# Kernel optimization log

Measured on AMD Instinct MI355X. Metric: run time of the kernel, lower is better.

Reference implementation:

```python
import jax, jax.numpy as jnp
import numpy as np

B, L, D = 4, 2048, 1024
DK, H = 64, 16
DFF = 4 * D
MASK_FILL = -2**15 + 1  # -32767, matches masked_fill value in source


def setup_inputs() -> dict:
    key = jax.random.key(0)
    ks = jax.random.split(key, 16)
    s = lambda fan_in: 1.0 / np.sqrt(fan_in)
    inp = {
        "x": jax.random.normal(ks[0], (B, L, D), dtype=jnp.float32),
        "maskPAD": jax.random.randint(ks[1], (B, L, L), 0, 2, dtype=jnp.int32),
        # attention projections (torch Linear layout: [out, in])
        "WQ_w": jax.random.uniform(ks[2], (H * DK, D), jnp.float32, -s(D), s(D)),
        "WQ_b": jnp.zeros((H * DK,), jnp.float32),
        "WK_w": jax.random.uniform(ks[3], (H * DK, D), jnp.float32, -s(D), s(D)),
        "WK_b": jnp.zeros((H * DK,), jnp.float32),
        "WV_w": jax.random.uniform(ks[4], (H * DK, D), jnp.float32, -s(D), s(D)),
        "WV_b": jnp.zeros((H * DK,), jnp.float32),
        "WO_w": jax.random.uniform(ks[5], (D, H * DK), jnp.float32, -s(H * DK), s(H * DK)),
        "WO_b": jnp.zeros((D,), jnp.float32),
        # FFN (pre-LN inside the FFN block)
        "ln_g": jnp.ones((D,), jnp.float32),
        "ln_b": jnp.zeros((D,), jnp.float32),
        "W1_w": jax.random.uniform(ks[6], (DFF, D), jnp.float32, -s(D), s(D)),
        "W1_b": jnp.zeros((DFF,), jnp.float32),
        "W2_w": jax.random.uniform(ks[7], (D, DFF), jnp.float32, -s(DFF), s(DFF)),
        "W2_b": jnp.zeros((D,), jnp.float32),
    }
    return inp


def _layernorm(x, g, b, eps=1e-5):
    mu = jnp.mean(x, axis=-1, keepdims=True)
    var = jnp.var(x, axis=-1, keepdims=True)
    return (x - mu) * jax.lax.rsqrt(var + eps) * g + b


def reference(x, maskPAD, WQ_w, WQ_b, WK_w, WK_b, WV_w, WV_b, WO_w, WO_b,
              ln_g, ln_b, W1_w, W1_b, W2_w, W2_b):
    # --- SelfAttention_PostLN (dropout = identity at eval) ---
    q = (jnp.einsum('bld,ed->ble', x, WQ_w) + WQ_b).reshape(B, L, H, DK).transpose(0, 2, 1, 3)
    k = (jnp.einsum('bld,ed->ble', x, WK_w) + WK_b).reshape(B, L, H, DK).transpose(0, 2, 1, 3)
    v = (jnp.einsum('bld,ed->ble', x, WV_w) + WV_b).reshape(B, L, H, DK).transpose(0, 2, 1, 3)
    scores = jnp.einsum('bhqd,bhkd->bhqk', q, k) / np.sqrt(DK).astype(np.float32)
    scores = jnp.where((maskPAD == 0)[:, None, :, :], jnp.float32(MASK_FILL), scores)
    alpha = jax.nn.softmax(scores, axis=-1)
    z = jnp.einsum('bhqk,bhkd->bhqd', alpha, v)  # [B,H,L,DK]
    z = z.transpose(0, 2, 1, 3).reshape(B, L, H * DK)
    z = jnp.einsum('ble,de->bld', z, WO_w) + WO_b
    # --- FFN_PreLN ---
    r = x + z                                    # residual 1 (dropout identity)
    h = _layernorm(r, ln_g, ln_b)
    h = jax.nn.relu(jnp.einsum('bld,fd->blf', h, W1_w) + W1_b)
    h = jnp.einsum('blf,df->bld', h, W2_w) + W2_b
    return r + h
```

## Files before the change

kernel.cpp:

```cpp
#include <hip/hip_runtime.h>

#define BD      4
#define LSEQ    2048
#define DMODEL  1024
#define HHEADS  16
#define DKK     64
#define DFFN    4096
#define MROWS   (BD*LSEQ)
#define QKS     2048

typedef float  f32x4  __attribute__((ext_vector_type(4)));
typedef float  f32x16 __attribute__((ext_vector_type(16)));
typedef __bf16 bf16x8 __attribute__((ext_vector_type(8)));
typedef unsigned short u16x8 __attribute__((ext_vector_type(8)));
typedef unsigned int   u32x4 __attribute__((ext_vector_type(4)));

__device__ inline unsigned short f2bf(float x) {
    union { float f; unsigned u; } c; c.f = x;
    unsigned r = c.u + 0x7FFFu + ((c.u >> 16) & 1u);
    return (unsigned short)(r >> 16);
}

__global__ void cast_bf16_k(const float* __restrict__ in,
                            unsigned short* __restrict__ out, long n) {
    long i = ((long)blockIdx.x * blockDim.x + threadIdx.x) * 4;
    long stride = (long)gridDim.x * blockDim.x * 4;
    for (; i < n; i += stride) {
        float4 v = *(const float4*)(in + i);
        ushort4 o;
        o.x = f2bf(v.x); o.y = f2bf(v.y); o.z = f2bf(v.z); o.w = f2bf(v.w);
        *(ushort4*)(out + i) = o;
    }
}

__global__ void concat3_k(const float* __restrict__ a, const float* __restrict__ b,
                          const float* __restrict__ c, float* __restrict__ o) {
    int i = blockIdx.x * 256 + threadIdx.x;
    if (i < 1024) { o[i] = a[i]; o[1024 + i] = b[i]; o[2048 + i] = c[i]; }
}

__global__ __launch_bounds__(256) void maskbits_k(const int* __restrict__ m,
                                                  unsigned long long* __restrict__ bits) {
    const long gw = ((long)blockIdx.x * blockDim.x + threadIdx.x) >> 6;
    const int lane = threadIdx.x & 63;
    const int b   = (int)(gw >> 16);
    const int rem = (int)gw & 65535;
    const int q = rem >> 5, kt = rem & 31;
    const int v = m[((size_t)(b*LSEQ + q))*LSEQ + kt*64 + lane];
    const unsigned long long bal = __ballot(v != 0);
    if (lane == 0) bits[((size_t)(b*32 + kt))*LSEQ + q] = bal;
}

__device__ inline void gload16(const void* g, void* l) {
    __builtin_amdgcn_global_load_lds(
        (const __attribute__((address_space(1))) void*)g,
        (__attribute__((address_space(3))) void*)l, 16, 0, 0);
}

#define BAR() { __builtin_amdgcn_sched_barrier(0); __builtin_amdgcn_s_barrier(); __builtin_amdgcn_sched_barrier(0); }

#define STAGE(XSEL, XPTR, h, tau, s)                                              \
  { const unsigned short* gs0 = (XPTR) + (size_t)((h)*128 + wid*8 + srow) * K + (tau)*64 + schk*8; \
    gload16(gs0, (void*)&sm[(s)][(XSEL)][(((h)*128 + wid*8)*64)]);                 \
    gload16(gs0 + (size_t)64*K, (void*)&sm[(s)][(XSEL)][(((h)*128 + 64 + wid*8)*64)]); }

#define LDA(dst, s, mi, kk) dst = *(const bf16x8*)(&sm[(s)][0][(wr*128 + (mi)*16 + r0)*64 + ((((kk)*4 + g) ^ (r0 & 7)) << 3)]);
#define LDB(dst, s, nj, kk) dst = *(const bf16x8*)(&sm[(s)][1][(wc*64  + (nj)*16 + r0)*64 + ((((kk)*4 + g) ^ (r0 & 7)) << 3)]);

#define PHASE_MFMA(q)                                                                                   \
    __builtin_amdgcn_s_setprio(1);                                                                      \
    _Pragma("unroll")                                                                                   \
    for (int nj = 0; nj < 4; ++nj) {                                                                    \
        acc[2*(q)][nj]   = __builtin_amdgcn_mfma_f32_16x16x32_bf16(af00, bq[nj][0], acc[2*(q)][nj],   0,0,0); \
        acc[2*(q)][nj]   = __builtin_amdgcn_mfma_f32_16x16x32_bf16(af01, bq[nj][1], acc[2*(q)][nj],   0,0,0); \
        acc[2*(q)+1][nj] = __builtin_amdgcn_mfma_f32_16x16x32_bf16(af10, bq[nj][0], acc[2*(q)+1][nj], 0,0,0); \
        acc[2*(q)+1][nj] = __builtin_amdgcn_mfma_f32_16x16x32_bf16(af11, bq[nj][1], acc[2*(q)+1][nj], 0,0,0); \
    }                                                                                                   \
    __builtin_amdgcn_s_setprio(0);

#define KTILE(s, tau)                                                        \
  {                                                                          \
    const int tp1 = (tau) + 1, tp2 = (tau) + 2;                              \
    bf16x8 bq[4][2];                                                         \
    bf16x8 af00, af01, af10, af11;                                           \
    _Pragma("unroll") for (int nj = 0; nj < 4; ++nj) {                       \
        LDB(bq[nj][0], s, nj, 0); LDB(bq[nj][1], s, nj, 1); }                \
    LDA(af00, s, 0, 0); LDA(af01, s, 0, 1);                                  \
    LDA(af10, s, 1, 0); LDA(af11, s, 1, 1);                                  \
    if (tp1 < NTT) { STAGE(0, Ab, 0, tp1, (s)^1); }                          \
    BAR(); PHASE_MFMA(0); BAR();                                             \
    LDA(af00, s, 2, 0); LDA(af01, s, 2, 1);                                  \
    LDA(af10, s, 3, 0); LDA(af11, s, 3, 1);                                  \
    if (tp1 < NTT) { STAGE(0, Ab, 1, tp1, (s)^1); }                          \
    if (tp2 < NTT) { STAGE(1, Bb, 0, tp2, (s)); }                            \
    BAR(); PHASE_MFMA(1); BAR();                                             \
    LDA(af00, s, 4, 0); LDA(af01, s, 4, 1);                                  \
    LDA(af10, s, 5, 0); LDA(af11, s, 5, 1);                                  \
    if (tp2 < NTT) { STAGE(1, Bb, 1, tp2, (s)); }                            \
    BAR(); PHASE_MFMA(2); BAR();                                             \
    LDA(af00, s, 6, 0); LDA(af01, s, 6, 1);                                  \
    LDA(af10, s, 7, 0); LDA(af11, s, 7, 1);                                  \
    if (tp2 < NTT)      { asm volatile("s_waitcnt vmcnt(4)" ::: "memory"); } \
    else if (tp1 < NTT) { asm volatile("s_waitcnt vmcnt(0)" ::: "memory"); } \
    BAR(); PHASE_MFMA(3); BAR();                                             \
  }

template<int MODE, int NTT>
__global__ __launch_bounds__(512, 1) void gemm8(const unsigned short* __restrict__ A,
                                                const unsigned short* __restrict__ B,
                                                const float* __restrict__ bias,
                                                unsigned short* __restrict__ Cout,
                                                int M, int N, int K, float scaleQ)
{
    __shared__ unsigned short sm[2][2][256*64];
    const int t   = threadIdx.x;
    const int wid = t >> 6, lane = t & 63;
    const int wr  = wid >> 2, wc = wid & 3;
    const int r0  = lane & 15, g = lane >> 4;

    const int nwg = gridDim.x;
    const int bid = (blockIdx.x & 7) * (nwg >> 3) + (blockIdx.x >> 3);
    const int ntn = N >> 8;
    const int bm  = (bid / ntn) << 8, bn = (bid % ntn) << 8;

    const int srow = lane >> 3;
    const int schk = (lane & 7) ^ srow;
    const unsigned short* Ab = A + (size_t)bm * K;
    const unsigned short* Bb = B + (size_t)bn * K;

    f32x4 acc[8][4] = {};

    STAGE(1, Bb, 0, 0, 0); STAGE(1, Bb, 1, 0, 0);
    STAGE(0, Ab, 0, 0, 0); STAGE(0, Ab, 1, 0, 0);
    STAGE(1, Bb, 0, 1, 1); STAGE(1, Bb, 1, 1, 1);
    asm volatile("s_waitcnt vmcnt(4)" ::: "memory");
    BAR();

#pragma unroll 1
    for (int i2 = 0; i2 < NTT/2; ++i2) {
        const int tau = 2*i2;
        KTILE(0, tau);
        KTILE(1, tau+1);
    }

#pragma unroll
    for (int mi = 0; mi < 8; ++mi) {
        const int row0 = bm + wr*128 + mi*16 + g*4;
#pragma unroll
        for (int nj = 0; nj < 4; ++nj) {
            const int col = bn + wc*64 + nj*16 + r0;
            const float bcol = bias[col];
#pragma unroll
            for (int rr = 0; rr < 4; ++rr) {
                float c = acc[mi][nj][rr] + bcol;
                if (MODE == 1) c = fmaxf(c, 0.f);
                Cout[(size_t)(row0 + rr) * N + col] = f2bf(c);
            }
        }
    }
}

#define STAGEA2(h, tau, s)                                                        \
  { const unsigned short* gs0 = Ab + (size_t)((h)*128 + wid*8 + srow) * K + (tau)*64 + schk*8; \
    gload16(gs0, (void*)&smA[(s)][(((h)*128 + wid*8)*64)]);                        \
    gload16(gs0 + (size_t)64*K, (void*)&smA[(s)][(((h)*128 + 64 + wid*8)*64)]); }

#define STAGEB2(tau, s)                                                           \
  { const unsigned short* gs0 = Bb + (size_t)(wid*8 + srow) * K + (tau)*64 + schk*8; \
    gload16(gs0, (void*)&smB[(s)][((wid*8)*64)]);                                  \
    gload16(gs0 + (size_t)64*K, (void*)&smB[(s)][((64 + wid*8)*64)]); }

#define LDA2(dst, s, mi, kk) dst = *(const bf16x8*)(&smA[(s)][(wr*128 + (mi)*16 + r0)*64 + ((((kk)*4 + g) ^ (r0 & 7)) << 3)]);
#define LDB2(dst, s, nj, kk) dst = *(const bf16x8*)(&smB[(s)][(wc*32  + (nj)*16 + r0)*64 + ((((kk)*4 + g) ^ (r0 & 7)) << 3)]);

#define PHASE_MFMA2X(q0)                                                                                \
    __builtin_amdgcn_s_setprio(1);                                                                      \
    _Pragma("unroll")                                                                                   \
    for (int mm = 0; mm < 4; ++mm) {                                                                    \
        acc[(q0)+mm][0] = __builtin_amdgcn_mfma_f32_16x16x32_bf16(aa[2*mm],   bq[0][0], acc[(q0)+mm][0], 0,0,0); \
        acc[(q0)+mm][0] = __builtin_amdgcn_mfma_f32_16x16x32_bf16(aa[2*mm+1], bq[0][1], acc[(q0)+mm][0], 0,0,0); \
        acc[(q0)+mm][1] = __builtin_amdgcn_mfma_f32_16x16x32_bf16(aa[2*mm],   bq[1][0], acc[(q0)+mm][1], 0,0,0); \
        acc[(q0)+mm][1] = __builtin_amdgcn_mfma_f32_16x16x32_bf16(aa[2*mm+1], bq[1][1], acc[(q0)+mm][1], 0,0,0); \
    }                                                                                                   \
    __builtin_amdgcn_s_setprio(0);

#define KTILE2(s, tau)                                                       \
  {                                                                          \
    const int tp1 = (tau) + 1, tp2 = (tau) + 2;                              \
    bf16x8 bq[2][2];                                                         \
    bf16x8 aa[8];                                                            \
    LDB2(bq[0][0], s, 0, 0); LDB2(bq[0][1], s, 0, 1);                        \
    LDB2(bq[1][0], s, 1, 0); LDB2(bq[1][1], s, 1, 1);                        \
    LDA2(aa[0], s, 0, 0); LDA2(aa[1], s, 0, 1);                              \
    LDA2(aa[2], s, 1, 0); LDA2(aa[3], s, 1, 1);                              \
    LDA2(aa[4], s, 2, 0); LDA2(aa[5], s, 2, 1);                              \
    LDA2(aa[6], s, 3, 0); LDA2(aa[7], s, 3, 1);                              \
    if (tp1 < NTT) { STAGEA2(0, tp1, (s)^1); }                               \
    BAR(); PHASE_MFMA2X(0); BAR();                                           \
    LDA2(aa[0], s, 4, 0); LDA2(aa[1], s, 4, 1);                              \
    LDA2(aa[2], s, 5, 0); LDA2(aa[3], s, 5, 1);                              \
    LDA2(aa[4], s, 6, 0); LDA2(aa[5], s, 6, 1);                              \
    LDA2(aa[6], s, 7, 0); LDA2(aa[7], s, 7, 1);                              \
    if (tp1 < NTT) { STAGEA2(1, tp1, (s)^1); }                               \
    if (tp2 < NTT) { STAGEB2(tp2, (s)); }                                    \
    if (tp2 < NTT)      { asm volatile("s_waitcnt vmcnt(2)" ::: "memory"); } \
    else if (tp1 < NTT) { asm volatile("s_waitcnt vmcnt(0)" ::: "memory"); } \
    BAR(); PHASE_MFMA2X(4); BAR();                                           \
  }

template<int MODE, int NTT>
__global__ __launch_bounds__(512, 1) void gemm8n(const unsigned short* __restrict__ A,
                                                 const unsigned short* __restrict__ B,
                                                 const float* __restrict__ bias,
                                                 const float* __restrict__ resid,
                                                 void* __restrict__ Cout,
                                                 unsigned short* __restrict__ vt,
                                                 int M, int N, int K, float scaleQ)
{
    __shared__ unsigned short smA[2][256*64];
    __shared__ unsigned short smB[2][128*64];
    const int t   = threadIdx.x;
    const int wid = t >> 6, lane = t & 63;
    const int wr  = wid >> 2, wc = wid & 3;
    const int r0  = lane & 15, g = lane >> 4;

    const int nwg = gridDim.x;
    const int bid = (blockIdx.x & 7) * (nwg >> 3) + (blockIdx.x >> 3);
    const int ntn = N >> 7;
    const int bm  = (bid / ntn) << 8, bn = (bid % ntn) << 7;

    const int srow = lane >> 3;
    const int schk = (lane & 7) ^ srow;
    const unsigned short* Ab = A + (size_t)bm * K;
    const unsigned short* Bb = B + (size_t)bn * K;

    f32x4 acc[8][2] = {};

    STAGEB2(0, 0);
    STAGEA2(0, 0, 0); STAGEA2(1, 0, 0);
    STAGEB2(1, 1);
    asm volatile("s_waitcnt vmcnt(2)" ::: "memory");
    BAR();

#pragma unroll 1
    for (int i2 = 0; i2 < NTT/2; ++i2) {
        const int tau = 2*i2;
        KTILE2(0, tau);
        KTILE2(1, tau+1);
    }

#pragma unroll
    for (int mi = 0; mi < 8; ++mi) {
        const int row0 = bm + wr*128 + mi*16 + g*4;
#pragma unroll
        for (int nj = 0; nj < 2; ++nj) {
            const int col = bn + wc*32 + nj*16 + r0;
            const float bcol = bias[col];
#pragma unroll
            for (int rr = 0; rr < 4; ++rr) {
                const int row = row0 + rr;
                if (MODE == 2) {
                    float c = acc[mi][nj][rr] + bcol;
                    ((float*)Cout)[(size_t)row * N + col] = c + resid[(size_t)row * N + col];
                }
            }
            if (MODE == 3) {
                if (col < 2048) {
                    const float sc = (col < 1024) ? scaleQ : 1.0f;
#pragma unroll
                    for (int rr = 0; rr < 4; ++rr)
                        ((unsigned short*)Cout)[(size_t)(row0 + rr) * QKS + col] =
                            f2bf((acc[mi][nj][rr] + bcol) * sc);
                } else {
                    const int vcol = col - 2048;
                    const int b = row0 >> 11, tok = row0 & 2047;
                    ushort4 h4;
                    h4.x = f2bf(acc[mi][nj][0] + bcol);
                    h4.y = f2bf(acc[mi][nj][1] + bcol);
                    h4.z = f2bf(acc[mi][nj][2] + bcol);
                    h4.w = f2bf(acc[mi][nj][3] + bcol);
                    *(ushort4*)&vt[((size_t)(b*1024 + vcol))*LSEQ + tok] = h4;
                }
            }
        }
    }
}

#define MFILL   (-47272.79f)
#define DEFTHR  (11.5415603f)
__global__ __launch_bounds__(256, 3) void attn_k(
    const unsigned short* __restrict__ QK,
    const unsigned short* __restrict__ VT,
    const unsigned long long* __restrict__ MBits,
    unsigned short* __restrict__ Z)
{
    __shared__ unsigned short Ks[2][64*64];
    __shared__ unsigned short Vs[2][64*64];
    __shared__ float Sc[4*32];

    const int t    = threadIdx.x;
    const int w    = t >> 6, lane = t & 63;
    const int q31  = lane & 31, hi = lane >> 5;

    const int bid = blockIdx.x;
    const int sw  = (bid & 7) * 128 + (bid >> 3);
    const int qt  = sw & 15, h = (sw >> 4) & 15, b = sw >> 8;
    const int qw  = qt * 128 + w * 32;

    const unsigned short* Qg = QK + ((size_t)(b*LSEQ + qw + q31))*QKS + h*DKK + hi*8;
    bf16x8 qf[4];
#pragma unroll
    for (int ds = 0; ds < 4; ++ds)
        qf[ds] = *(const bf16x8*)(Qg + ds*16);

    const int srow = w*8 + (lane>>3);
    const int schk = (lane & 7) ^ (srow & 7);
    const unsigned short* kP = QK + ((size_t)(b*LSEQ))*QKS + 1024 + h*DKK
                                  + (size_t)srow*QKS + schk*8;
    const unsigned short* vP = VT + ((size_t)(b*1024 + h*DKK))*LSEQ
                                  + (size_t)srow*LSEQ + schk*8;
    const unsigned long long* mP = MBits + ((size_t)(b*32))*LSEQ + (qw + q31);

    float m_r = MFILL, l_r = 0.f;
    f32x16 z0, z1;
#pragma unroll
    for (int r = 0; r < 16; ++r) { z0[r] = 0.f; z1[r] = 0.f; }

    gload16(kP,           &Ks[0][w*512]);
    gload16(kP + 32*QKS,  &Ks[0][w*512] + 2048);
    gload16(vP,           &Vs[0][w*512]);
    gload16(vP + 32*LSEQ, &Vs[0][w*512] + 2048);
    unsigned long long mw = *mP;
    kP += 64*QKS; vP += 64; mP += LSEQ;

    for (int kt = 0; kt < LSEQ/64; ++kt) {
        const int cur = kt & 1;
        __syncthreads();

        gload16(kP,           &Ks[cur^1][w*512]);
        gload16(kP + 32*QKS,  &Ks[cur^1][w*512] + 2048);
        gload16(vP,           &Vs[cur^1][w*512]);
        gload16(vP + 32*LSEQ, &Vs[cur^1][w*512] + 2048);
        const unsigned long long mwn = (kt < LSEQ/64 - 1) ? *mP : mw;
        kP += 64*QKS; vP += 64; mP += LSEQ;

        const unsigned long long sh = mw >> (hi*4);
        const unsigned md0 = (unsigned)sh, md1 = (unsigned)(sh >> 32);

        f32x16 s0, s1;
#pragma unroll
        for (int r = 0; r < 16; ++r) { s0[r] = 0.f; s1[r] = 0.f; }
        __builtin_amdgcn_s_setprio(1);
#pragma unroll
        for (int ds = 0; ds < 4; ++ds) {
            const int slot = ((ds*2 + hi) ^ (q31 & 7)) << 3;
            bf16x8 kf0 = *(const bf16x8*)(&Ks[cur][ q31     *64 + slot]);
            bf16x8 kf1 = *(const bf16x8*)(&Ks[cur][(32+q31)*64 + slot]);
            s0 = __builtin_amdgcn_mfma_f32_32x32x16_bf16(kf0, qf[ds], s0, 0, 0, 0);
            s1 = __builtin_amdgcn_mfma_f32_32x32x16_bf16(kf1, qf[ds], s1, 0, 0, 0);
        }
        __builtin_amdgcn_s_setprio(0);

        float a8[16];
#pragma unroll
        for (int r = 0; r < 16; ++r) a8[r] = fmaxf(s0[r], s1[r]);
        {
            float t0 = fmaxf(fmaxf(a8[0],  a8[1]),  a8[2]);
            float t1 = fmaxf(fmaxf(a8[3],  a8[4]),  a8[5]);
            float t2 = fmaxf(fmaxf(a8[6],  a8[7]),  a8[8]);
            float t3 = fmaxf(fmaxf(a8[9],  a8[10]), a8[11]);
            float t4 = fmaxf(fmaxf(a8[12], a8[13]), a8[14]);
            float u0 = fmaxf(fmaxf(t0, t1), t2);
            float u1 = fmaxf(fmaxf(t3, t4), a8[15]);
            float tm = fmaxf(u0, u1);
            float ta = tm, tb = tm;
            asm volatile("v_permlane32_swap_b32 %0, %1" : "+v"(ta), "+v"(tb));
            tm = fmaxf(tm, hi ? ta : tb);

            if (__any(tm > m_r + DEFTHR)) {
                const float nm   = fmaxf(m_r, tm);
                const float corr = exp2f(m_r - nm);
                Sc[w*32 + q31] = corr;
                l_r *= corr;
                m_r  = nm;
#pragma unroll
                for (int r = 0; r < 16; ++r) {
                    const int row = (r & 3) + 8*(r >> 2) + 4*hi;
                    const float cr = Sc[w*32 + row];
                    z0[r] *= cr; z1[r] *= cr;
                }
            }
        }

#pragma unroll
        for (int r = 0; r < 16; ++r) {
            const int kb = (r & 3) + 8*(r >> 2);
            s0[r] = exp2f(s0[r] - m_r);
            s1[r] = exp2f(s1[r] - m_r);
            if (!((md0 >> kb) & 1)) s0[r] = 0.f;
            if (!((md1 >> kb) & 1)) s1[r] = 0.f;
        }
        float r4[8];
#pragma unroll
        for (int r = 0; r < 8; ++r)
            r4[r] = (s0[2*r] + s0[2*r+1]) + (s1[2*r] + s1[2*r+1]);
        float rs = ((r4[0]+r4[1]) + (r4[2]+r4[3])) + ((r4[4]+r4[5]) + (r4[6]+r4[7]));
        {
            float ra = rs, rb = rs;
            asm volatile("v_permlane32_swap_b32 %0, %1" : "+v"(ra), "+v"(rb));
            rs += hi ? ra : rb;
        }
        l_r += rs;

        __builtin_amdgcn_s_setprio(1);
#pragma unroll
        for (int half = 0; half < 2; ++half) {
#pragma unroll
            for (int sub = 0; sub < 2; ++sub) {
                const int base = sub*8;
                unsigned wa, wb, wc2, wd;
                float p0 = half ? s1[base+0] : s0[base+0];
                float p1 = half ? s1[base+1] : s0[base+1];
                float p2 = half ? s1[base+2] : s0[base+2];
                float p3 = half ? s1[base+3] : s0[base+3];
                float p4 = half ? s1[base+4] : s0[base+4];
                float p5 = half ? s1[base+5] : s0[base+5];
                float p6 = half ? s1[base+6] : s0[base+6];
                float p7 = half ? s1[base+7] : s0[base+7];
                asm("v_cvt_pk_bf16_f32 %0, %1, %2" : "=v"(wa) : "v"(p0), "v"(p1));
                asm("v_cvt_pk_bf16_f32 %0, %1, %2" : "=v"(wb) : "v"(p4), "v"(p5));
                asm("v_cvt_pk_bf16_f32 %0, %1, %2" : "=v"(wc2) : "v"(p2), "v"(p3));
                asm("v_cvt_pk_bf16_f32 %0, %1, %2" : "=v"(wd) : "v"(p6), "v"(p7));
                asm volatile("v_permlane32_swap_b32 %0, %1" : "+v"(wa), "+v"(wb));
                asm volatile("v_permlane32_swap_b32 %0, %1" : "+v"(wc2), "+v"(wd));
                u32x4 pu; pu[0] = wa; pu[1] = wc2; pu[2] = wb; pu[3] = wd;
                bf16x8 pa = __builtin_bit_cast(bf16x8, pu);
                const int ks = half*2 + sub;
                const int slot = ((ks*2 + hi) ^ (q31 & 7)) << 3;
                bf16x8 vf0 = *(const bf16x8*)(&Vs[cur][ q31     *64 + slot]);
                bf16x8 vf1 = *(const bf16x8*)(&Vs[cur][(32+q31)*64 + slot]);
                z0 = __builtin_amdgcn_mfma_f32_32x32x16_bf16(pa, vf0, z0, 0, 0, 0);
                z1 = __builtin_amdgcn_mfma_f32_32x32x16_bf16(pa, vf1, z1, 0, 0, 0);
            }
        }
        __builtin_amdgcn_s_setprio(0);

        mw = mwn;
    }

    Sc[w*32 + q31] = l_r;
    unsigned short* Zb = Z + ((size_t)(b*LSEQ + qw))*DMODEL + h*DKK + q31;
#pragma unroll
    for (int r = 0; r < 16; ++r) {
        const int row = (r & 3) + 8*(r >> 2) + 4*hi;
        const float rl = 1.0f / Sc[w*32 + row];
        Zb[(size_t)row*DMODEL]      = f2bf(z0[r] * rl);
        Zb[(size_t)row*DMODEL + 32] = f2bf(z1[r] * rl);
    }
}

__global__ __launch_bounds__(256) void ln_k(const float* __restrict__ r,
                                            const float* __restrict__ gam,
                                            const float* __restrict__ bet,
                                            unsigned short* __restrict__ out)
{
    const int row = blockIdx.x;
    const int t = threadIdx.x;
    const float* rp = r + (size_t)row * DMODEL;
    float4 v = *(const float4*)(rp + t*4);
    float s  = v.x + v.y + v.z + v.w;
    float s2 = v.x*v.x + v.y*v.y + v.z*v.z + v.w*v.w;
#pragma unroll
    for (int off = 32; off >= 1; off >>= 1) {
        s  += __shfl_xor(s,  off);
        s2 += __shfl_xor(s2, off);
    }
    __shared__ float red[8];
    const int wv = t >> 6;
    if ((t & 63) == 0) { red[wv] = s; red[4 + wv] = s2; }
    __syncthreads();
    s  = red[0] + red[1] + red[2] + red[3];
    s2 = red[4] + red[5] + red[6] + red[7];
    const float mu   = s  * (1.f/DMODEL);
    const float var  = s2 * (1.f/DMODEL) - mu*mu;
    const float rstd = rsqrtf(var + 1e-5f);
    float4 gv = *(const float4*)(gam + t*4);
    float4 bv = *(const float4*)(bet + t*4);
    ushort4 o;
    o.x = f2bf((v.x - mu)*rstd*gv.x + bv.x);
    o.y = f2bf((v.y - mu)*rstd*gv.y + bv.y);
    o.z = f2bf((v.z - mu)*rstd*gv.z + bv.z);
    o.w = f2bf((v.w - mu)*rstd*gv.w + bv.w);
    *(ushort4*)(out + (size_t)row * DMODEL + t*4) = o;
}

extern "C" void kernel_launch(void* const* d_in, const int* in_sizes, int n_in,
                              void* d_out, int out_size, void* d_ws, size_t ws_size,
                              hipStream_t stream)
{
    const float* x    = (const float*)d_in[0];
    const int*   mask = (const int*)  d_in[1];
    const float* WQ_w = (const float*)d_in[2];
    const float* WQ_b = (const float*)d_in[3];
    const float* WK_w = (const float*)d_in[4];
    const float* WK_b = (const float*)d_in[5];
    const float* WV_w = (const float*)d_in[6];
    const float* WV_b = (const float*)d_in[7];
    const float* WO_w = (const float*)d_in[8];
    const float* WO_b = (const float*)d_in[9];
    const float* ln_g = (const float*)d_in[10];
    const float* ln_b = (const float*)d_in[11];
    const float* W1_w = (const float*)d_in[12];
    const float* W1_b = (const float*)d_in[13];
    const float* W2_w = (const float*)d_in[14];
    const float* W2_b = (const float*)d_in[15];
    float* out = (float*)d_out;

    char* w = (char*)d_ws;
    const size_t MB = 1024*1024;
    unsigned short* qk   = (unsigned short*)(w + 0*MB);
    unsigned short* vtb  = (unsigned short*)(w + 32*MB);
    unsigned short* shr  = (unsigned short*)(w + 64*MB);
    float*          rb   = (float*)         (w + 80*MB);
    unsigned short* wqkv = (unsigned short*)(w + 112*MB);
    unsigned short* wob  = (unsigned short*)(w + 118*MB);
    unsigned short* w1b  = (unsigned short*)(w + 120*MB);
    unsigned short* w2b  = (unsigned short*)(w + 128*MB);
    unsigned long long* mbits = (unsigned long long*)(w + 136*MB);
    float* bqkv = (float*)rb;
    unsigned short* xb   = shr;
    unsigned short* Zb   = shr;
    unsigned short* hln  = shr;
    unsigned short* hmid = (unsigned short*)(w + 0*MB);

    cast_bf16_k<<<2048, 256, 0, stream>>>(x,    xb,   (long)MROWS*DMODEL);
    cast_bf16_k<<<512,  256, 0, stream>>>(WQ_w, wqkv,               (long)DMODEL*DMODEL);
    cast_bf16_k<<<512,  256, 0, stream>>>(WK_w, wqkv + 1024*1024,   (long)DMODEL*DMODEL);
    cast_bf16_k<<<512,  256, 0, stream>>>(WV_w, wqkv + 2*1024*1024, (long)DMODEL*DMODEL);
    cast_bf16_k<<<512,  256, 0, stream>>>(WO_w, wob,  (long)DMODEL*DMODEL);
    cast_bf16_k<<<2048, 256, 0, stream>>>(W1_w, w1b,  (long)DFFN*DMODEL);
    cast_bf16_k<<<2048, 256, 0, stream>>>(W2_w, w2b,  (long)DMODEL*DFFN);
    maskbits_k<<<65536, 256, 0, stream>>>(mask, mbits);
    concat3_k<<<4, 256, 0, stream>>>(WQ_b, WK_b, WV_b, bqkv);

    gemm8n<3, 16><<<dim3(768), dim3(512), 0, stream>>>(xb, wqkv, bqkv, nullptr, qk, vtb,
                                                       MROWS, 3072, DMODEL, 0.18033688f);
    attn_k<<<dim3(1024), dim3(256), 0, stream>>>(qk, vtb, mbits, Zb);
    gemm8n<2, 16><<<dim3(256), dim3(512), 0, stream>>>(Zb, wob, WO_b, x, rb, nullptr,
                                                       MROWS, DMODEL, DMODEL, 1.0f);
    ln_k<<<MROWS, 256, 0, stream>>>(rb, ln_g, ln_b, hln);
    gemm8<1, 16><<<dim3(512), dim3(512), 0, stream>>>(hln, w1b, W1_b, hmid,
                                                      MROWS, DFFN, DMODEL, 1.0f);
    gemm8n<2, 64><<<dim3(256), dim3(512), 0, stream>>>(hmid, w2b, W2_b, rb, out, nullptr,
                                                       MROWS, DMODEL, DFFN, 1.0f);
}
```

Baseline: 472.8 us.

## Merge weight casts into one kernel and move QKV/W2 GEMMs to 256x256 tiles

The six separate weight-cast launches become one grid-stride kernel that converts all weight matrices. The QKV projection and the W2 down-projection move from the 256x128-tile gemm8n kernel to the 256x256-tile gemm8 kernel, which gains the residual and QKV/V-transpose epilogues. Larger tiles raise arithmetic intensity and cut redundant operand loads. The cost is fewer workgroups: 384 for QKV and only 128 for W2, which may underfill the 256 CUs on MI355X.

After: 474.3 us. About the same (+0.3%).

```diff
diff --git a/kernel.cpp b/kernel.cpp
--- a/kernel.cpp
+++ b/kernel.cpp
@@ -30,6 +30,29 @@
         ushort4 o;
         o.x = f2bf(v.x); o.y = f2bf(v.y); o.z = f2bf(v.z); o.w = f2bf(v.w);
         *(ushort4*)(out + i) = o;
+    }
+}
+
+__global__ void cast_weights_k(const float* __restrict__ wq, const float* __restrict__ wk,
+                               const float* __restrict__ wv, const float* __restrict__ wo,
+                               const float* __restrict__ w1, const float* __restrict__ w2,
+                               unsigned short* __restrict__ dqkv, unsigned short* __restrict__ dwo,
+                               unsigned short* __restrict__ dw1, unsigned short* __restrict__ dw2) {
+    const long M1 = 1024*1024;
+    long i = ((long)blockIdx.x * blockDim.x + threadIdx.x) * 4;
+    long stride = (long)gridDim.x * blockDim.x * 4;
+    for (; i < 12*M1; i += stride) {
+        const float* src; unsigned short* dst;
+        if      (i <   M1) { src = wq + i;          dst = dqkv + i; }
+        else if (i < 2*M1) { src = wk + (i-M1);     dst = dqkv + i; }
+        else if (i < 3*M1) { src = wv + (i-2*M1);   dst = dqkv + i; }
+        else if (i < 4*M1) { src = wo + (i-3*M1);   dst = dwo + (i-3*M1); }
+        else if (i < 8*M1) { src = w1 + (i-4*M1);   dst = dw1 + (i-4*M1); }
+        else               { src = w2 + (i-8*M1);   dst = dw2 + (i-8*M1); }
+        float4 v = *(const float4*)src;
+        ushort4 o;
+        o.x = f2bf(v.x); o.y = f2bf(v.y); o.z = f2bf(v.z); o.w = f2bf(v.w);
+        *(ushort4*)dst = o;
     }
 }
 
@@ -109,7 +132,9 @@
 __global__ __launch_bounds__(512, 1) void gemm8(const unsigned short* __restrict__ A,
                                                 const unsigned short* __restrict__ B,
                                                 const float* __restrict__ bias,
-                                                unsigned short* __restrict__ Cout,
+                                                const float* __restrict__ resid,
+                                                void* __restrict__ Cout,
+                                                unsigned short* __restrict__ vt,
                                                 int M, int N, int K, float scaleQ)
 {
     __shared__ unsigned short sm[2][2][256*64];
@@ -150,11 +175,35 @@
         for (int nj = 0; nj < 4; ++nj) {
             const int col = bn + wc*64 + nj*16 + r0;
             const float bcol = bias[col];
-#pragma unroll
-            for (int rr = 0; rr < 4; ++rr) {
-                float c = acc[mi][nj][rr] + bcol;
-                if (MODE == 1) c = fmaxf(c, 0.f);
-                Cout[(size_t)(row0 + rr) * N + col] = f2bf(c);
+            if (MODE == 1) {
+#pragma unroll
+                for (int rr = 0; rr < 4; ++rr) {
+                    float c = fmaxf(acc[mi][nj][rr] + bcol, 0.f);
+                    ((unsigned short*)Cout)[(size_t)(row0 + rr) * N + col] = f2bf(c);
+                }
+            } else if (MODE == 2) {
+#pragma unroll
+                for (int rr = 0; rr < 4; ++rr) {
+                    const size_t idx = (size_t)(row0 + rr) * N + col;
+                    ((float*)Cout)[idx] = acc[mi][nj][rr] + bcol + resid[idx];
+                }
+            } else if (MODE == 3) {
+                if (col < 2048) {
+                    const float sc = (col < 1024) ? scaleQ : 1.0f;
+#pragma unroll
+                    for (int rr = 0; rr < 4; ++rr)
+                        ((unsigned short*)Cout)[(size_t)(row0 + rr) * QKS + col] =
+                            f2bf((acc[mi][nj][rr] + bcol) * sc);
+                } else {
+                    const int vcol = col - 2048;
+                    const int b = row0 >> 11, tok = row0 & 2047;
+                    ushort4 h4;
+                    h4.x = f2bf(acc[mi][nj][0] + bcol);
+                    h4.y = f2bf(acc[mi][nj][1] + bcol);
+                    h4.z = f2bf(acc[mi][nj][2] + bcol);
+                    h4.w = f2bf(acc[mi][nj][3] + bcol);
+                    *(ushort4*)&vt[((size_t)(b*1024 + vcol))*LSEQ + tok] = h4;
+                }
             }
         }
     }
@@ -214,8 +263,7 @@
                                                  const float* __restrict__ bias,
                                                  const float* __restrict__ resid,
                                                  void* __restrict__ Cout,
-                                                 unsigned short* __restrict__ vt,
-                                                 int M, int N, int K, float scaleQ)
+                                                 int M, int N, int K)
 {
     __shared__ unsigned short smA[2][256*64];
     __shared__ unsigned short smB[2][128*64];
@@ -262,24 +310,6 @@
                 if (MODE == 2) {
                     float c = acc[mi][nj][rr] + bcol;
                     ((float*)Cout)[(size_t)row * N + col] = c + resid[(size_t)row * N + col];
-                }
-            }
-            if (MODE == 3) {
-                if (col < 2048) {
-                    const float sc = (col < 1024) ? scaleQ : 1.0f;
-#pragma unroll
-                    for (int rr = 0; rr < 4; ++rr)
-                        ((unsigned short*)Cout)[(size_t)(row0 + rr) * QKS + col] =
-                            f2bf((acc[mi][nj][rr] + bcol) * sc);
-                } else {
-                    const int vcol = col - 2048;
-                    const int b = row0 >> 11, tok = row0 & 2047;
-                    ushort4 h4;
-                    h4.x = f2bf(acc[mi][nj][0] + bcol);
-                    h4.y = f2bf(acc[mi][nj][1] + bcol);
-                    h4.z = f2bf(acc[mi][nj][2] + bcol);
-                    h4.w = f2bf(acc[mi][nj][3] + bcol);
-                    *(ushort4*)&vt[((size_t)(b*1024 + vcol))*LSEQ + tok] = h4;
                 }
             }
         }
@@ -533,24 +563,20 @@
     unsigned short* hln  = shr;
     unsigned short* hmid = (unsigned short*)(w + 0*MB);
 
-    cast_bf16_k<<<2048, 256, 0, stream>>>(x,    xb,   (long)MROWS*DMODEL);
-    cast_bf16_k<<<512,  256, 0, stream>>>(WQ_w, wqkv,               (long)DMODEL*DMODEL);
-    cast_bf16_k<<<512,  256, 0, stream>>>(WK_w, wqkv + 1024*1024,   (long)DMODEL*DMODEL);
-    cast_bf16_k<<<512,  256, 0, stream>>>(WV_w, wqkv + 2*1024*1024, (long)DMODEL*DMODEL);
-    cast_bf16_k<<<512,  256, 0, stream>>>(WO_w, wob,  (long)DMODEL*DMODEL);
-    cast_bf16_k<<<2048, 256, 0, stream>>>(W1_w, w1b,  (long)DFFN*DMODEL);
-    cast_bf16_k<<<2048, 256, 0, stream>>>(W2_w, w2b,  (long)DMODEL*DFFN);
+    cast_bf16_k<<<2048, 256, 0, stream>>>(x, xb, (long)MROWS*DMODEL);
+    cast_weights_k<<<2048, 256, 0, stream>>>(WQ_w, WK_w, WV_w, WO_w, W1_w, W2_w,
+                                             wqkv, wob, w1b, w2b);
     maskbits_k<<<65536, 256, 0, stream>>>(mask, mbits);
     concat3_k<<<4, 256, 0, stream>>>(WQ_b, WK_b, WV_b, bqkv);
 
-    gemm8n<3, 16><<<dim3(768), dim3(512), 0, stream>>>(xb, wqkv, bqkv, nullptr, qk, vtb,
-                                                       MROWS, 3072, DMODEL, 0.18033688f);
+    gemm8<3, 16><<<dim3(384), dim3(512), 0, stream>>>(xb, wqkv, bqkv, nullptr, qk, vtb,
+                                                      MROWS, 3072, DMODEL, 0.18033688f);
     attn_k<<<dim3(1024), dim3(256), 0, stream>>>(qk, vtb, mbits, Zb);
-    gemm8n<2, 16><<<dim3(256), dim3(512), 0, stream>>>(Zb, wob, WO_b, x, rb, nullptr,
-                                                       MROWS, DMODEL, DMODEL, 1.0f);
+    gemm8n<2, 16><<<dim3(256), dim3(512), 0, stream>>>(Zb, wob, WO_b, x, rb,
+                                                       MROWS, DMODEL, DMODEL);
     ln_k<<<MROWS, 256, 0, stream>>>(rb, ln_g, ln_b, hln);
-    gemm8<1, 16><<<dim3(512), dim3(512), 0, stream>>>(hln, w1b, W1_b, hmid,
+    gemm8<1, 16><<<dim3(512), dim3(512), 0, stream>>>(hln, w1b, W1_b, nullptr, hmid, nullptr,
                                                       MROWS, DFFN, DMODEL, 1.0f);
-    gemm8n<2, 64><<<dim3(256), dim3(512), 0, stream>>>(hmid, w2b, W2_b, rb, out, nullptr,
-                                                       MROWS, DMODEL, DFFN, 1.0f);
-}
+    gemm8<2, 64><<<dim3(128), dim3(512), 0, stream>>>(hmid, w2b, W2_b, rb, out, nullptr,
+                                                      MROWS, DMODEL, DFFN, 1.0f);
+}
```
